# Optimization experiments

Hardware: AMD Instinct MI355X
Metric: run time of the kernel (lower is better)

The kernel has to match this reference:

```python
import jax, jax.numpy as jnp
import numpy as np

BATCH, N_SEQS, SEQ_LEN, D_IN, D_OUT = 8, 4, 2048, 512, 512
LN_EPS = 1e-5


def setup_inputs() -> dict:
    key = jax.random.key(0)
    ks = jax.random.split(key, 6)
    s_in = 1.0 / np.sqrt(D_IN)
    s_out = 1.0 / np.sqrt(D_OUT)
    return {
        "x": jax.random.normal(ks[0], (BATCH, N_SEQS * SEQ_LEN * D_IN), dtype=jnp.float32),
        "Wq": jax.random.normal(ks[1], (D_OUT, D_IN), dtype=jnp.float32) * s_in,
        "Wk": jax.random.normal(ks[2], (D_OUT, D_IN), dtype=jnp.float32) * s_in,
        "Wv": jax.random.normal(ks[3], (D_OUT, D_IN), dtype=jnp.float32) * s_in,
        "Wo": jax.random.normal(ks[4], (D_OUT, D_OUT), dtype=jnp.float32) * s_out,
        "bo": jnp.zeros((D_OUT,), dtype=jnp.float32),
        "gamma": jnp.ones((D_OUT,), dtype=jnp.float32),
        "beta": jnp.zeros((D_OUT,), dtype=jnp.float32),
    }


def _phi(x):
    # positive feature map: elu(x) + 1
    return jax.nn.elu(x) + 1.0


def reference(x, Wq, Wk, Wv, Wo, bo, gamma, beta):
    batch = x.shape[0]
    xs = x.reshape(batch * N_SEQS, SEQ_LEN, D_IN)  # [B*L, S, d_in]
    Q = _phi(jnp.einsum('bsi,oi->bso', xs, Wq))     # [B*L, S, d_out]
    K = _phi(jnp.einsum('bsi,oi->bso', xs, Wk))
    V = jnp.einsum('bsi,oi->bso', xs, Wv)
    kv = jnp.einsum('bsd,bse->bde', K, V)           # [B*L, d_out, d_out]
    num = jnp.einsum('bsd,bde->bse', Q, kv)         # [B*L, S, d_out]
    k_sum = K.sum(axis=1, keepdims=True)            # [B*L, 1, d_out]
    den = jnp.maximum((Q * k_sum).sum(axis=-1, keepdims=True), 1e-6)
    out = num / den
    y = jnp.einsum('bse,oe->bso', out, Wo) + bo + out  # out_proj + residual
    mu = y.mean(axis=-1, keepdims=True)
    var = ((y - mu) ** 2).mean(axis=-1, keepdims=True)
    y = (y - mu) * jax.lax.rsqrt(var + LN_EPS) * gamma + beta
    return y.reshape(batch, -1)
```

## Files before the change

kernel.cpp:

```cpp
#include <hip/hip_runtime.h>
#include <cstdint>

typedef __bf16 bf16x8 __attribute__((ext_vector_type(8)));
typedef float  f32x4  __attribute__((ext_vector_type(4)));

#define SEQS   32
#define SLEN   2048
#define DIM    512
#define MROWS  65536

static __device__ __forceinline__ void load_lds16(const void* g, void* l) {
  __builtin_amdgcn_global_load_lds(
      (const __attribute__((address_space(1))) void*)(uintptr_t)g,
      (__attribute__((address_space(3))) void*)(uintptr_t)l,
      16, 0, 0);
}

static __device__ __forceinline__ unsigned short bfbits(float f) {
  __bf16 h = (__bf16)f;
  unsigned short u;
  __builtin_memcpy(&u, &h, 2);
  return u;
}

static __device__ __forceinline__ void gemm_core(
    const __bf16* __restrict__ A, int lda, int arow0,
    const __bf16* __restrict__ B, int ldb, int brow0,
    int K, __bf16* Asm, __bf16* Bsm, f32x4 (&acc)[4][4])
{
  const int tid  = threadIdx.x;
  const int wave = tid >> 6;
  const int lane = tid & 63;
  const int wr = wave >> 1, wc = wave & 1;
  const int lr = lane & 15, kq = lane >> 4;

  for (int kt = 0; kt < K; kt += 64) {
#pragma unroll
    for (int q = 0; q < 4; ++q) {
      const int L  = q * 4096 + tid * 16;
      const int r  = L >> 7;
      const int sl = (L >> 4) & 7;
      const int c  = ((sl ^ (r & 7)) << 3);
      load_lds16(A + (size_t)(arow0 + r) * lda + (kt + c),
                 (char*)Asm + q * 4096 + wave * 1024);
      load_lds16(B + (size_t)(brow0 + r) * ldb + (kt + c),
                 (char*)Bsm + q * 4096 + wave * 1024);
    }
    __syncthreads();

    bf16x8 af[2][4], bfr[2][4];
#pragma unroll
    for (int kk = 0; kk < 2; ++kk)
#pragma unroll
      for (int i = 0; i < 4; ++i) {
        const int rA = wr * 64 + i * 16 + lr;
        af[kk][i] = *reinterpret_cast<const bf16x8*>(
            (char*)Asm + rA * 128 + ((((kk * 4 + kq) ^ (rA & 7))) << 4));
        const int rB = wc * 64 + i * 16 + lr;
        bfr[kk][i] = *reinterpret_cast<const bf16x8*>(
            (char*)Bsm + rB * 128 + ((((kk * 4 + kq) ^ (rB & 7))) << 4));
      }
#pragma unroll
    for (int kk = 0; kk < 2; ++kk)
#pragma unroll
      for (int i = 0; i < 4; ++i)
#pragma unroll
        for (int j = 0; j < 4; ++j)
          acc[i][j] = __builtin_amdgcn_mfma_f32_16x16x32_bf16(
              af[kk][i], bfr[kk][j], acc[i][j], 0, 0, 0);
    __syncthreads();
  }
}


__global__ __launch_bounds__(256) void castall_kernel(
    const float* __restrict__ x, __bf16* __restrict__ xb,
    const float* __restrict__ wq, const float* __restrict__ wk,
    const float* __restrict__ wv, const float* __restrict__ wo,
    __bf16* __restrict__ wqb, __bf16* __restrict__ wkb,
    __bf16* __restrict__ wvb, __bf16* __restrict__ wob)
{
  const int X8 = MROWS * DIM / 8;
  const int W8 = DIM * DIM / 8;
  const int total = X8 + 4 * W8;
  int i = blockIdx.x * blockDim.x + threadIdx.x;
  const int stride = gridDim.x * blockDim.x;
  for (; i < total; i += stride) {
    const float* src; __bf16* dst; int off;
    if (i < X8) { src = x; dst = xb; off = i; }
    else {
      const int wsel = (i - X8) / W8;
      off = (i - X8) - wsel * W8;
      src = (wsel == 0) ? wq : (wsel == 1) ? wk : (wsel == 2) ? wv : wo;
      dst = (wsel == 0) ? wqb : (wsel == 1) ? wkb : (wsel == 2) ? wvb : wob;
    }
    const float4* p = reinterpret_cast<const float4*>(src + (size_t)off * 8);
    float4 a = p[0], b2 = p[1];
    float vals[8] = {a.x, a.y, a.z, a.w, b2.x, b2.y, b2.z, b2.w};
    uint32_t w[4];
#pragma unroll
    for (int t = 0; t < 4; ++t)
      w[t] = (uint32_t)bfbits(vals[2 * t]) | ((uint32_t)bfbits(vals[2 * t + 1]) << 16);
    uint4 o; o.x = w[0]; o.y = w[1]; o.z = w[2]; o.w = w[3];
    *reinterpret_cast<uint4*>(dst + (size_t)off * 8) = o;
  }
}

__global__ __launch_bounds__(512, 1) void qkv_kernel(
    const __bf16* __restrict__ xb,
    const __bf16* __restrict__ Wqb, const __bf16* __restrict__ Wkb,
    const __bf16* __restrict__ Wvb,
    __bf16* __restrict__ Q, __bf16* __restrict__ KT, __bf16* __restrict__ VT,
    float* __restrict__ ksum)
{
  __shared__ __align__(16) __bf16 As[2][256 * 64];
  __shared__ __align__(16) __bf16 Bs[2][256 * 64];
  const int b = blockIdx.x;
  const int xcd = b & 7, loc = b >> 3;
  const int brow = (loc / 6) * 8 + xcd;
  const int inner = loc % 6;
  const int z = inner >> 1, bcol = inner & 1;
  const __bf16* W = (z == 0) ? Wqb : (z == 1) ? Wkb : Wvb;

  const int tid = threadIdx.x, wave = tid >> 6, lane = tid & 63;
  const int wr = wave >> 2, wn = wave & 3;
  const int lr = lane & 15, kq = lane >> 4;

  const __bf16* Abase = xb + (size_t)(brow * 256) * DIM;
  const __bf16* Bbase = W + (size_t)(bcol * 256) * DIM;

  auto stage = [&](int s, int kt) {
#pragma unroll
    for (int q = 0; q < 4; ++q) {
      const int L  = q * 8192 + tid * 16;
      const int r  = L >> 7;
      const int sl = (L >> 4) & 7;
      const int c  = ((sl ^ (r & 7)) << 3);
      load_lds16(Abase + (size_t)r * DIM + (kt + c),
                 (char*)(&As[s][0]) + q * 8192 + wave * 1024);
      load_lds16(Bbase + (size_t)r * DIM + (kt + c),
                 (char*)(&Bs[s][0]) + q * 8192 + wave * 1024);
    }
  };

  f32x4 acc[8][4] = {};

  stage(0, 0);
  __syncthreads();
  for (int t = 0; t < 8; ++t) {
    const int cur = t & 1;
    if (t < 7) stage(cur ^ 1, (t + 1) * 64);
#pragma unroll
    for (int kk = 0; kk < 2; ++kk) {
      bf16x8 bfr[4], af[8];
#pragma unroll
      for (int j = 0; j < 4; ++j) {
        const int rB = wn * 64 + j * 16 + lr;
        bfr[j] = *reinterpret_cast<const bf16x8*>(
            (const char*)(&Bs[cur][0]) + rB * 128 + (((kk * 4 + kq) ^ (rB & 7)) << 4));
      }
#pragma unroll
      for (int i = 0; i < 8; ++i) {
        const int rA = wr * 128 + i * 16 + lr;
        af[i] = *reinterpret_cast<const bf16x8*>(
            (const char*)(&As[cur][0]) + rA * 128 + (((kk * 4 + kq) ^ (rA & 7)) << 4));
      }
#pragma unroll
      for (int i = 0; i < 8; ++i)
#pragma unroll
        for (int j = 0; j < 4; ++j)
          acc[i][j] = __builtin_amdgcn_mfma_f32_16x16x32_bf16(af[i], bfr[j], acc[i][j], 0, 0, 0);
    }
    __syncthreads();
  }

  const int m00 = brow * 256 + wr * 128 + kq * 4;
  const int n00 = bcol * 256 + wn * 64 + lr;
  if (z == 0) {
#pragma unroll
    for (int i = 0; i < 8; ++i)
#pragma unroll
      for (int j = 0; j < 4; ++j) {
        const int n = n00 + j * 16;
#pragma unroll
        for (int r = 0; r < 4; ++r) {
          const int m = m00 + i * 16 + r;
          float v = acc[i][j][r];
          v = (v > 0.f) ? (v + 1.f) : __expf(v);
          Q[(size_t)m * DIM + n] = (__bf16)v;
        }
      }
  } else {
    __bf16* T = (z == 1) ? KT : VT;
    const int seq = (brow * 256) >> 11;
    float ks[4] = {0.f, 0.f, 0.f, 0.f};
#pragma unroll
    for (int i = 0; i < 8; ++i) {
      const int mb = m00 + i * 16;
      const int s0 = mb & 2047;
#pragma unroll
      for (int j = 0; j < 4; ++j) {
        const int d = n00 + j * 16;
        unsigned short h[4];
#pragma unroll
        for (int r = 0; r < 4; ++r) {
          float v = acc[i][j][r];
          if (z == 1) { v = (v > 0.f) ? (v + 1.f) : __expf(v); ks[j] += v; }
          h[r] = bfbits(v);
        }
        uint2 u;
        u.x = (uint32_t)h[0] | ((uint32_t)h[1] << 16);
        u.y = (uint32_t)h[2] | ((uint32_t)h[3] << 16);
        *reinterpret_cast<uint2*>(T + ((size_t)(seq * DIM + d) << 11) + s0) = u;
      }
    }
    if (z == 1) {
#pragma unroll
      for (int j = 0; j < 4; ++j) {
        float p = ks[j];
        p += __shfl_xor(p, 16, 64);
        p += __shfl_xor(p, 32, 64);
        if (kq == 0) atomicAdd(&ksum[seq * DIM + n00 + j * 16], p);
      }
    }
  }
}

__global__ __launch_bounds__(256) void kv_kernel(
    const __bf16* __restrict__ VT, const __bf16* __restrict__ KT,
    __bf16* __restrict__ kvT)
{
  __shared__ __align__(16) __bf16 Asm[128 * 64];
  __shared__ __align__(16) __bf16 Bsm[128 * 64];
  const int b = blockIdx.x;
  const int xcd = b & 7, loc = b >> 3;
  const int seq = (loc >> 4) * 8 + xcd;
  const int inner = loc & 15;
  const int bxx = inner >> 2, byy = inner & 3;
  const __bf16* A = VT + (size_t)seq * DIM * SLEN;
  const __bf16* B = KT + (size_t)seq * DIM * SLEN;
  f32x4 acc[4][4] = {};
  gemm_core(A, SLEN, bxx * 128, B, SLEN, byy * 128, SLEN, Asm, Bsm, acc);

  const int tid = threadIdx.x, wave = tid >> 6, lane = tid & 63;
  const int wr = wave >> 1, wc = wave & 1, lr = lane & 15, kq = lane >> 4;
  const int m0 = bxx * 128 + wr * 64 + kq * 4;
  const int n0 = byy * 128 + wc * 64 + lr;
  __bf16* C = kvT + (size_t)seq * DIM * DIM;
#pragma unroll
  for (int i = 0; i < 4; ++i)
#pragma unroll
    for (int j = 0; j < 4; ++j)
#pragma unroll
      for (int r = 0; r < 4; ++r)
        C[(size_t)(m0 + i * 16 + r) * DIM + (n0 + j * 16)] = (__bf16)acc[i][j][r];
}

__global__ __launch_bounds__(512, 1) void num_kernel(
    const __bf16* __restrict__ Q, const __bf16* __restrict__ kvT,
    const float* __restrict__ ksum, __bf16* __restrict__ out)
{
  __shared__ __align__(16) __bf16 As[2][256 * 64];
  __shared__ __align__(16) __bf16 Bs[2][256 * 64];
  __shared__ __align__(16) __bf16 ks_lds[512];
  const int b = blockIdx.x;
  const int xcd = b & 7, loc = b >> 3;
  const int seq = (loc >> 4) * 8 + xcd;
  const int inner = loc & 15;
  const int brow = inner >> 1, bcol = inner & 1;
  const size_t grow0 = (size_t)seq * SLEN + brow * 256;

  const int tid = threadIdx.x, wave = tid >> 6, lane = tid & 63;
  const int wr = wave >> 2, wn = wave & 3;
  const int lr = lane & 15, kq = lane >> 4;

  const __bf16* Abase = Q + grow0 * DIM;
  const __bf16* Bbase = kvT + (size_t)seq * DIM * DIM + (size_t)(bcol * 256) * DIM;

  auto stage = [&](int s, int kt) {
#pragma unroll
    for (int q = 0; q < 4; ++q) {
      const int L  = q * 8192 + tid * 16;
      const int r  = L >> 7;
      const int sl = (L >> 4) & 7;
      const int c  = ((sl ^ (r & 7)) << 3);
      load_lds16(Abase + (size_t)r * DIM + (kt + c),
                 (char*)(&As[s][0]) + q * 8192 + wave * 1024);
      load_lds16(Bbase + (size_t)r * DIM + (kt + c),
                 (char*)(&Bs[s][0]) + q * 8192 + wave * 1024);
    }
  };

  f32x4 acc[8][4] = {};
  f32x4 accd[8] = {};

  ks_lds[tid] = (__bf16)ksum[seq * DIM + tid];
  stage(0, 0);
  __syncthreads();
  for (int t = 0; t < 8; ++t) {
    const int cur = t & 1;
    if (t < 7) stage(cur ^ 1, (t + 1) * 64);
#pragma unroll
    for (int kk = 0; kk < 2; ++kk) {
      bf16x8 bfr[4], af[8];
      const bf16x8 ksf = *reinterpret_cast<const bf16x8*>(
          &ks_lds[t * 64 + kk * 32 + kq * 8]);
#pragma unroll
      for (int j = 0; j < 4; ++j) {
        const int rB = wn * 64 + j * 16 + lr;
        bfr[j] = *reinterpret_cast<const bf16x8*>(
            (const char*)(&Bs[cur][0]) + rB * 128 + (((kk * 4 + kq) ^ (rB & 7)) << 4));
      }
#pragma unroll
      for (int i = 0; i < 8; ++i) {
        const int rA = wr * 128 + i * 16 + lr;
        af[i] = *reinterpret_cast<const bf16x8*>(
            (const char*)(&As[cur][0]) + rA * 128 + (((kk * 4 + kq) ^ (rA & 7)) << 4));
      }
#pragma unroll
      for (int i = 0; i < 8; ++i) {
#pragma unroll
        for (int j = 0; j < 4; ++j)
          acc[i][j] = __builtin_amdgcn_mfma_f32_16x16x32_bf16(af[i], bfr[j], acc[i][j], 0, 0, 0);
        accd[i] = __builtin_amdgcn_mfma_f32_16x16x32_bf16(af[i], ksf, accd[i], 0, 0, 0);
      }
    }
    __syncthreads();
  }

  const size_t g0 = grow0 + wr * 128 + kq * 4;
  const int n00 = bcol * 256 + wn * 64 + lr;
#pragma unroll
  for (int i = 0; i < 8; ++i) {
    float rd[4];
#pragma unroll
    for (int r = 0; r < 4; ++r)
      rd[r] = 1.f / fmaxf(accd[i][r], 1e-6f);
#pragma unroll
    for (int j = 0; j < 4; ++j)
#pragma unroll
      for (int r = 0; r < 4; ++r)
        out[(g0 + i * 16 + r) * DIM + (n00 + j * 16)] =
            (__bf16)(acc[i][j][r] * rd[r]);
  }
}

__global__ __launch_bounds__(512, 1) void final_kernel(
    const __bf16* __restrict__ outb, const __bf16* __restrict__ Wob,
    const float* __restrict__ bo, const float* __restrict__ gamma,
    const float* __restrict__ beta, float* __restrict__ y)
{
  __shared__ __align__(16) __bf16 Asm[2][128 * 32];
  __shared__ __align__(16) __bf16 Bsm[2][512 * 32];
  __shared__ float redS[4][128], redSS[4][128];
  const int tid = threadIdx.x, wave = tid >> 6, lane = tid & 63;
  const int Wr = wave >> 2, Wc = wave & 3;
  const int lr = lane & 15, kq = lane >> 4;
  const int brow = blockIdx.x;
  f32x4 acc[4][8] = {};

  auto stage = [&](int s, int kt) {
    {
      const int L = tid * 16;
      const int r = L >> 6, sl = (L >> 4) & 3;
      const int c = ((sl ^ ((r >> 1) & 3)) << 3);
      load_lds16(outb + (size_t)(brow * 128 + r) * DIM + (kt + c),
                 (char*)(&Asm[s][0]) + wave * 1024);
    }
#pragma unroll
    for (int q = 0; q < 4; ++q) {
      const int L = q * 8192 + tid * 16;
      const int r = L >> 6, sl = (L >> 4) & 3;
      const int c = ((sl ^ ((r >> 1) & 3)) << 3);
      load_lds16(Wob + (size_t)r * DIM + (kt + c),
                 (char*)(&Bsm[s][0]) + q * 8192 + wave * 1024);
    }
  };

  stage(0, 0);
  __syncthreads();
  for (int t = 0; t < 16; ++t) {
    const int cur = t & 1;
    if (t < 15) stage(cur ^ 1, (t + 1) * 32);
    bf16x8 af[4];
#pragma unroll
    for (int i = 0; i < 4; ++i) {
      const int rA = Wr * 64 + i * 16 + lr;
      af[i] = *reinterpret_cast<const bf16x8*>(
          (char*)(&Asm[cur][0]) + rA * 64 + ((kq ^ ((rA >> 1) & 3)) << 4));
    }
#pragma unroll
    for (int j = 0; j < 8; ++j) {
      const int rB = Wc * 128 + j * 16 + lr;
      bf16x8 bf = *reinterpret_cast<const bf16x8*>(
          (char*)(&Bsm[cur][0]) + rB * 64 + ((kq ^ ((rB >> 1) & 3)) << 4));
#pragma unroll
      for (int i = 0; i < 4; ++i)
        acc[i][j] = __builtin_amdgcn_mfma_f32_16x16x32_bf16(af[i], bf, acc[i][j], 0, 0, 0);
    }
    __syncthreads();
  }

  const int m0g = brow * 128;
  float sA[4][4] = {{0.f}}, ssA[4][4] = {{0.f}};
#pragma unroll
  for (int j = 0; j < 8; ++j) {
    const int n = Wc * 128 + j * 16 + lr;
    const float bon = bo[n];
#pragma unroll
    for (int i = 0; i < 4; ++i) {
      const int mb = m0g + Wr * 64 + i * 16 + kq * 4;
#pragma unroll
      for (int r = 0; r < 4; ++r) {
        float v = acc[i][j][r] + bon + (float)outb[(size_t)(mb + r) * DIM + n];
        acc[i][j][r] = v;
        sA[i][r] += v; ssA[i][r] += v * v;
      }
    }
  }
#pragma unroll
  for (int i = 0; i < 4; ++i)
#pragma unroll
    for (int r = 0; r < 4; ++r) {
      float s = sA[i][r], ss = ssA[i][r];
#pragma unroll
      for (int off = 1; off <= 8; off <<= 1) {
        s  += __shfl_xor(s,  off, 64);
        ss += __shfl_xor(ss, off, 64);
      }
      if (lr == 0) {
        const int ml = Wr * 64 + i * 16 + kq * 4 + r;
        redS[Wc][ml] = s; redSS[Wc][ml] = ss;
      }
    }
  __syncthreads();
  float mu_[4][4], rs_[4][4];
#pragma unroll
  for (int i = 0; i < 4; ++i)
#pragma unroll
    for (int r = 0; r < 4; ++r) {
      const int ml = Wr * 64 + i * 16 + kq * 4 + r;
      const float S  = redS[0][ml] + redS[1][ml] + redS[2][ml] + redS[3][ml];
      const float SS = redSS[0][ml] + redSS[1][ml] + redSS[2][ml] + redSS[3][ml];
      const float mu = S * (1.f / 512.f);
      const float var = SS * (1.f / 512.f) - mu * mu;
      mu_[i][r] = mu;
      rs_[i][r] = rsqrtf(var + 1e-5f);
    }
#pragma unroll
  for (int j = 0; j < 8; ++j) {
    const int n = Wc * 128 + j * 16 + lr;
    const float g = gamma[n], bb = beta[n];
#pragma unroll
    for (int i = 0; i < 4; ++i) {
      const int mb = m0g + Wr * 64 + i * 16 + kq * 4;
#pragma unroll
      for (int r = 0; r < 4; ++r)
        y[(size_t)(mb + r) * DIM + n] = (acc[i][j][r] - mu_[i][r]) * rs_[i][r] * g + bb;
    }
  }
}

extern "C" void kernel_launch(void* const* d_in, const int* in_sizes, int n_in,
                              void* d_out, int out_size, void* d_ws, size_t ws_size,
                              hipStream_t stream)
{
  const float* x     = (const float*)d_in[0];
  const float* Wq    = (const float*)d_in[1];
  const float* Wk    = (const float*)d_in[2];
  const float* Wv    = (const float*)d_in[3];
  const float* Wo    = (const float*)d_in[4];
  const float* bo    = (const float*)d_in[5];
  const float* gamma = (const float*)d_in[6];
  const float* beta  = (const float*)d_in[7];
  float* outp = (float*)d_out;

  char* ws = (char*)d_ws;
  const size_t SZ = 67108864;
  __bf16* xb   = (__bf16*)(ws + 0);
  __bf16* Q    = (__bf16*)(ws + SZ);
  __bf16* KT   = (__bf16*)(ws + 2 * SZ);
  __bf16* VT   = (__bf16*)(ws + 3 * SZ);
  __bf16* kvT  = (__bf16*)(ws + 4 * SZ);
  __bf16* Wqb  = (__bf16*)(ws + 4 * SZ + 16777216);
  __bf16* Wkb  = Wqb + 262144;
  __bf16* Wvb  = Wkb + 262144;
  __bf16* Wob  = Wvb + 262144;
  float*  ksum = (float*)(Wob + 262144);

  hipMemsetAsync(ksum, 0, SEQS * DIM * sizeof(float), stream);
  castall_kernel<<<4224, 256, 0, stream>>>(x, xb, Wq, Wk, Wv, Wo,
                                           Wqb, Wkb, Wvb, Wob);

  qkv_kernel<<<1536, 512, 0, stream>>>(xb, Wqb, Wkb, Wvb, Q, KT, VT, ksum);
  kv_kernel<<<512, 256, 0, stream>>>(VT, KT, kvT);
  num_kernel<<<512, 512, 0, stream>>>(Q, kvT, ksum, xb );
  final_kernel<<<512, 512, 0, stream>>>(xb, Wob, bo, gamma, beta, outp);
}
```

Measured before the change: 375.1 us.

## Double-buffer kv_kernel with 128x256 tiles and 512-thread blocks

Rewrites the K^T V per-sequence GEMM to use a 128x256 output tile per 512-thread block with LDS double buffering, so the next K-slice's global-to-LDS load is issued before computing the current one. The grid halves to 256 blocks and the shared gemm_core helper is removed. This aims to hide load latency and improve reuse of the A tile. The cost is more LDS per block, one block per CU, and fewer blocks than CUs' worth of parallel waves in some configurations.

```diff
diff --git a/kernel.cpp b/kernel.cpp
--- a/kernel.cpp
+++ b/kernel.cpp
@@ -21,55 +21,6 @@
   unsigned short u;
   __builtin_memcpy(&u, &h, 2);
   return u;
-}
-
-static __device__ __forceinline__ void gemm_core(
-    const __bf16* __restrict__ A, int lda, int arow0,
-    const __bf16* __restrict__ B, int ldb, int brow0,
-    int K, __bf16* Asm, __bf16* Bsm, f32x4 (&acc)[4][4])
-{
-  const int tid  = threadIdx.x;
-  const int wave = tid >> 6;
-  const int lane = tid & 63;
-  const int wr = wave >> 1, wc = wave & 1;
-  const int lr = lane & 15, kq = lane >> 4;
-
-  for (int kt = 0; kt < K; kt += 64) {
-#pragma unroll
-    for (int q = 0; q < 4; ++q) {
-      const int L  = q * 4096 + tid * 16;
-      const int r  = L >> 7;
-      const int sl = (L >> 4) & 7;
-      const int c  = ((sl ^ (r & 7)) << 3);
-      load_lds16(A + (size_t)(arow0 + r) * lda + (kt + c),
-                 (char*)Asm + q * 4096 + wave * 1024);
-      load_lds16(B + (size_t)(brow0 + r) * ldb + (kt + c),
-                 (char*)Bsm + q * 4096 + wave * 1024);
-    }
-    __syncthreads();
-
-    bf16x8 af[2][4], bfr[2][4];
-#pragma unroll
-    for (int kk = 0; kk < 2; ++kk)
-#pragma unroll
-      for (int i = 0; i < 4; ++i) {
-        const int rA = wr * 64 + i * 16 + lr;
-        af[kk][i] = *reinterpret_cast<const bf16x8*>(
-            (char*)Asm + rA * 128 + ((((kk * 4 + kq) ^ (rA & 7))) << 4));
-        const int rB = wc * 64 + i * 16 + lr;
-        bfr[kk][i] = *reinterpret_cast<const bf16x8*>(
-            (char*)Bsm + rB * 128 + ((((kk * 4 + kq) ^ (rB & 7))) << 4));
-      }
-#pragma unroll
-    for (int kk = 0; kk < 2; ++kk)
-#pragma unroll
-      for (int i = 0; i < 4; ++i)
-#pragma unroll
-        for (int j = 0; j < 4; ++j)
-          acc[i][j] = __builtin_amdgcn_mfma_f32_16x16x32_bf16(
-              af[kk][i], bfr[kk][j], acc[i][j], 0, 0, 0);
-    __syncthreads();
-  }
 }
 
 
@@ -226,26 +177,79 @@
   }
 }
 
-__global__ __launch_bounds__(256) void kv_kernel(
+__global__ __launch_bounds__(512, 1) void kv_kernel(
     const __bf16* __restrict__ VT, const __bf16* __restrict__ KT,
     __bf16* __restrict__ kvT)
 {
-  __shared__ __align__(16) __bf16 Asm[128 * 64];
-  __shared__ __align__(16) __bf16 Bsm[128 * 64];
+  __shared__ __align__(16) __bf16 As[2][128 * 64];
+  __shared__ __align__(16) __bf16 Bs[2][256 * 64];
   const int b = blockIdx.x;
   const int xcd = b & 7, loc = b >> 3;
-  const int seq = (loc >> 4) * 8 + xcd;
-  const int inner = loc & 15;
-  const int bxx = inner >> 2, byy = inner & 3;
-  const __bf16* A = VT + (size_t)seq * DIM * SLEN;
-  const __bf16* B = KT + (size_t)seq * DIM * SLEN;
+  const int seq = (loc >> 3) * 8 + xcd;
+  const int inner = loc & 7;
+  const int mt = inner >> 1, nt = inner & 1;
+
+  const int tid = threadIdx.x, wave = tid >> 6, lane = tid & 63;
+  const int wr = wave >> 2, wn = wave & 3;
+  const int lr = lane & 15, kq = lane >> 4;
+
+  const __bf16* Abase = VT + (size_t)seq * DIM * SLEN + (size_t)(mt * 128) * SLEN;
+  const __bf16* Bbase = KT + (size_t)seq * DIM * SLEN + (size_t)(nt * 256) * SLEN;
+
+  auto stage = [&](int s, int kt) {
+#pragma unroll
+    for (int q = 0; q < 2; ++q) {
+      const int L  = q * 8192 + tid * 16;
+      const int r  = L >> 7;
+      const int sl = (L >> 4) & 7;
+      const int c  = ((sl ^ (r & 7)) << 3);
+      load_lds16(Abase + (size_t)r * SLEN + (kt + c),
+                 (char*)(&As[s][0]) + q * 8192 + wave * 1024);
+    }
+#pragma unroll
+    for (int q = 0; q < 4; ++q) {
+      const int L  = q * 8192 + tid * 16;
+      const int r  = L >> 7;
+      const int sl = (L >> 4) & 7;
+      const int c  = ((sl ^ (r & 7)) << 3);
+      load_lds16(Bbase + (size_t)r * SLEN + (kt + c),
+                 (char*)(&Bs[s][0]) + q * 8192 + wave * 1024);
+    }
+  };
+
   f32x4 acc[4][4] = {};
-  gemm_core(A, SLEN, bxx * 128, B, SLEN, byy * 128, SLEN, Asm, Bsm, acc);
-
-  const int tid = threadIdx.x, wave = tid >> 6, lane = tid & 63;
-  const int wr = wave >> 1, wc = wave & 1, lr = lane & 15, kq = lane >> 4;
-  const int m0 = bxx * 128 + wr * 64 + kq * 4;
-  const int n0 = byy * 128 + wc * 64 + lr;
+
+  stage(0, 0);
+  __syncthreads();
+  for (int t = 0; t < 32; ++t) {
+    const int cur = t & 1;
+    if (t < 31) stage(cur ^ 1, (t + 1) * 64);
+#pragma unroll
+    for (int kk = 0; kk < 2; ++kk) {
+      bf16x8 bfr[4], af[4];
+#pragma unroll
+      for (int j = 0; j < 4; ++j) {
+        const int rB = wn * 64 + j * 16 + lr;
+        bfr[j] = *reinterpret_cast<const bf16x8*>(
+            (const char*)(&Bs[cur][0]) + rB * 128 + (((kk * 4 + kq) ^ (rB & 7)) << 4));
+      }
+#pragma unroll
+      for (int i = 0; i < 4; ++i) {
+        const int rA = wr * 64 + i * 16 + lr;
+        af[i] = *reinterpret_cast<const bf16x8*>(
+            (const char*)(&As[cur][0]) + rA * 128 + (((kk * 4 + kq) ^ (rA & 7)) << 4));
+      }
+#pragma unroll
+      for (int i = 0; i < 4; ++i)
+#pragma unroll
+        for (int j = 0; j < 4; ++j)
+          acc[i][j] = __builtin_amdgcn_mfma_f32_16x16x32_bf16(af[i], bfr[j], acc[i][j], 0, 0, 0);
+    }
+    __syncthreads();
+  }
+
+  const int m0 = mt * 128 + wr * 64 + kq * 4;
+  const int n0 = nt * 256 + wn * 64 + lr;
   __bf16* C = kvT + (size_t)seq * DIM * DIM;
 #pragma unroll
   for (int i = 0; i < 4; ++i)
@@ -493,7 +497,7 @@
                                            Wqb, Wkb, Wvb, Wob);
 
   qkv_kernel<<<1536, 512, 0, stream>>>(xb, Wqb, Wkb, Wvb, Q, KT, VT, ksum);
-  kv_kernel<<<512, 256, 0, stream>>>(VT, KT, kvT);
+  kv_kernel<<<256, 512, 0, stream>>>(VT, KT, kvT);
   num_kernel<<<512, 512, 0, stream>>>(Q, kvT, ksum, xb );
   final_kernel<<<512, 512, 0, stream>>>(xb, Wob, bo, gamma, beta, outp);
 }
```

After: 373.7 us (median of 2 runs). No clear change (-0.4%).
